# Optimization experiments

Measured on AMD Instinct MI355X. Metric: run time of the kernel, lower is better.

## Reference

```python
import jax, jax.numpy as jnp
import numpy as np
from jax import lax

B = 64            # batch size
IMG = 128         # image H=W
C_IN = 3          # channels (also conv kernel size in original code)
Q_DIM = 11
A_DIM = 10
CONV = [24, 24, 24, 24]
KS = 3
EPS = 1e-5
G_IN = (CONV[-1] + 2) * 2 + Q_DIM  # 63


def _lin_init(key, fin, fout):
    kw, kb = jax.random.split(key)
    w = jax.random.normal(kw, (fin, fout), jnp.float32) / np.sqrt(fin).astype(np.float32)
    b = jax.random.normal(kb, (fout,), jnp.float32) * 0.01
    return w, b


def _conv_init(key, cin, cout):
    kw, kb = jax.random.split(key)
    w = jax.random.normal(kw, (cout, cin, KS, KS), jnp.float32) / np.sqrt(cin * KS * KS).astype(np.float32)
    b = jax.random.normal(kb, (cout,), jnp.float32) * 0.01
    return w, b


def setup_inputs() -> dict:
    key = jax.random.key(0)
    ks = jax.random.split(key, 16)
    inp = {
        'img': jax.random.normal(ks[0], (B, C_IN, IMG, IMG), jnp.float32),
        'q': jax.random.normal(ks[1], (B, Q_DIM), jnp.float32),
    }
    cins = [C_IN] + CONV[:-1]
    for li in range(4):
        w, b = _conv_init(ks[2 + li], cins[li], CONV[li])
        inp[f'cw{li+1}'], inp[f'cb{li+1}'] = w, b
        inp[f'bg{li+1}'] = jnp.ones((CONV[li],), jnp.float32)
        inp[f'bb{li+1}'] = jnp.zeros((CONV[li],), jnp.float32)
    gins = [G_IN, 256, 256, 256]
    for li in range(4):
        w, b = _lin_init(ks[6 + li], gins[li], 256)
        inp[f'gw{li+1}'], inp[f'gb{li+1}'] = w, b
    fins, fouts = [256, 256, 256], [256, 256, A_DIM]
    for li in range(3):
        w, b = _lin_init(ks[10 + li], fins[li], fouts[li])
        inp[f'fw{li+1}'], inp[f'fb{li+1}'] = w, b
    return inp


def _conv_block(x, w, b, g, bb):
    # conv(stride=2, pad=1) -> relu -> batchnorm (train-mode batch stats)
    x = lax.conv_general_dilated(x, w, (2, 2), [(1, 1), (1, 1)],
                                 dimension_numbers=('NCHW', 'OIHW', 'NCHW'))
    x = jax.nn.relu(x + b[None, :, None, None])
    m = jnp.mean(x, axis=(0, 2, 3), keepdims=True)
    v = jnp.var(x, axis=(0, 2, 3), keepdims=True)
    return g[None, :, None, None] * (x - m) * jax.lax.rsqrt(v + EPS) + bb[None, :, None, None]


def _forward(img, q,
             cw1, cb1, bg1, bb1, cw2, cb2, bg2, bb2,
             cw3, cb3, bg3, bb3, cw4, cb4, bg4, bb4,
             gw1, gb1, gw2, gb2, gw3, gb3, gw4, gb4,
             fw1, fb1, fw2, fb2, fw3, fb3):
    x = _conv_block(img, cw1, cb1, bg1, bb1)
    x = _conv_block(x, cw2, cb2, bg2, bb2)
    x = _conv_block(x, cw3, cb3, bg3, bb3)
    x = _conv_block(x, cw4, cb4, bg4, bb4)        # [B, K, d, d]
    d = x.shape[2]
    N = d * d
    Kc = x.shape[1]
    # objects: o at flat index i corresponds to pixel (i//d, i%d) -> row-major reshape
    objs = x.reshape(B, Kc, N).transpose(0, 2, 1)           # [B, N, K]
    idx = jnp.arange(N)
    coords = jnp.stack([(idx // d).astype(jnp.float32) / d,
                        (idx % d).astype(jnp.float32) / d], axis=1)  # [N, 2]
    o = jnp.concatenate([objs, jnp.broadcast_to(coords[None], (B, N, 2))], axis=-1)  # [B, N, K+2]
    F = Kc + 2
    oi = jnp.broadcast_to(o[:, :, None, :], (B, N, N, F))
    oj = jnp.broadcast_to(o[:, None, :, :], (B, N, N, F))
    qb = jnp.broadcast_to(q[:, None, None, :], (B, N, N, Q_DIM))
    pair = jnp.concatenate([oi, oj, qb], axis=-1)           # [B, N, N, 2F+Q]
    h = jax.nn.relu(jnp.einsum('bijf,fh->bijh', pair, gw1) + gb1)
    h = jax.nn.relu(h @ gw2 + gb2)
    h = jax.nn.relu(h @ gw3 + gb3)
    h = jax.nn.relu(h @ gw4 + gb4)
    g = jnp.mean(h, axis=(1, 2))                            # mean over all N*N pairs -> [B, 256]
    # f_phi (dropout as identity / eval mode)
    g = jax.nn.relu(g @ fw1 + fb1)
    g = jax.nn.relu(g @ fw2 + fb2)
    logits = g @ fw3 + fb3
    return logits


def reference(img, q,
              cw1, cb1, bg1, bb1, cw2, cb2, bg2, bb2,
              cw3, cb3, bg3, bb3, cw4, cb4, bg4, bb4,
              gw1, gb1, gw2, gb2, gw3, gb3, gw4, gb4,
              fw1, fb1, fw2, fb2, fw3, fb3):
    return _forward(img, q,
                    cw1, cb1, bg1, bb1, cw2, cb2, bg2, bb2,
                    cw3, cb3, bg3, bb3, cw4, cb4, bg4, bb4,
                    gw1, gb1, gw2, gb2, gw3, gb3, gw4, gb4,
                    fw1, fb1, fw2, fb2, fw3, fb3)
```

## Files before the change

kernel.cpp:

```cpp
#include <hip/hip_runtime.h>
#include <hip/hip_bf16.h>

#define EPS_BN 1e-5f

typedef __bf16 bf16_t;
typedef __bf16 bf16x8 __attribute__((ext_vector_type(8)));
typedef __bf16 bf16x4 __attribute__((ext_vector_type(4)));
typedef float fx4 __attribute__((ext_vector_type(4)));
typedef float floatx16 __attribute__((ext_vector_type(16)));

__global__ __launch_bounds__(256) void c1prep_kernel(
    const float* __restrict__ img, const float* __restrict__ w,
    const float* __restrict__ bias, float* __restrict__ out,
    float* __restrict__ part_out,
    const float* __restrict__ q, const float* __restrict__ gw1,
    const float* __restrict__ gb1, const float* __restrict__ g2,
    const float* __restrict__ g3, const float* __restrict__ g4,
    const float* __restrict__ gb2, const float* __restrict__ gb3,
    float* __restrict__ wq, bf16_t* __restrict__ wpack,
    float* __restrict__ biaspack)
{
    int t = threadIdx.x;
    if (blockIdx.x >= 2048) {
        int blk = blockIdx.x - 2048;
        {
            float acc = gb1[t];
            #pragma unroll
            for (int d = 0; d < 11; d++)
                acc = fmaf(q[blk * 11 + d], gw1[(52 + d) * 256 + t], acc);
            wq[blk * 256 + t] = acc;
        }
        if (blk == 0) {
            for (int idx = t; idx < 512; idx += 256) {
                int layer = idx >> 8;
                int rem = idx & 255;
                int cg = rem >> 5, l2 = (rem >> 4) & 1, reg = rem & 15;
                int c = cg * 32 + (reg & 3) + 8 * (reg >> 2) + 4 * l2;
                biaspack[idx] = (layer ? gb3 : gb2)[c];
            }
        }
        for (int f = blk * 384 + t; f < blk * 384 + 384; f += 256) {
            int lane = f & 63;
            int kt = (f >> 6) & 15;
            int cg = (f >> 10) & 7;
            int layer = f >> 13;
            const float* gw = (layer == 0) ? g2 : ((layer == 1) ? g3 : g4);
            int col = (cg << 5) + (lane & 31);
            int kb = kt * 16 + (lane >> 5) * 8;
            bf16x8 o;
            #pragma unroll
            for (int e = 0; e < 8; e++)
                o[e] = (bf16_t)gw[(kb + e) * 256 + col];
            *(bf16x8*)&wpack[(size_t)f * 8] = o;
        }
        return;
    }
    __shared__ float tin[3][7][130];
    __shared__ float red[4][24];
    int b = blockIdx.x / 32, tile = blockIdx.x % 32;
    int oy0 = tile * 2;
    int iyb = 2 * oy0 - 1;
    #pragma unroll 2
    for (int idx = t; idx < 3 * 7 * 130; idx += 256) {
        int rx = idx % 130;
        int rem = idx / 130;
        int ry = rem % 7;
        int ci = rem / 7;
        int iy = iyb + ry, ix = rx - 1;
        float v = 0.f;
        if ((unsigned)iy < 128u && (unsigned)ix < 128u)
            v = img[(b * 3 + ci) * 16384 + iy * 128 + ix];
        tin[ci][ry][rx] = v;
    }
    __syncthreads();
    int ox = t % 64;
    int oyl = (t / 64) % 2;
    int cog = t / 128;
    const float* wp = w + cog * 12 * 27;
    float acc[12];
    #pragma unroll
    for (int r = 0; r < 12; r++) acc[r] = bias[cog * 12 + r];
    #pragma unroll
    for (int ci = 0; ci < 3; ci++)
        #pragma unroll
        for (int ky = 0; ky < 3; ky++)
            #pragma unroll
            for (int kx = 0; kx < 3; kx++) {
                float v = tin[ci][2 * oyl + ky][2 * ox + kx];
                #pragma unroll
                for (int r = 0; r < 12; r++)
                    acc[r] = fmaf(v, wp[(r * 3 + ci) * 9 + ky * 3 + kx], acc[r]);
            }
    int oy = oy0 + oyl;
    float s1[12], s2[12];
    #pragma unroll
    for (int r = 0; r < 12; r++) {
        float v = fmaxf(acc[r], 0.f);
        out[((b * 24 + cog * 12 + r) * 64 + oy) * 64 + ox] = v;
        s1[r] = v;
        s2[r] = v * v;
    }
    int lane = t & 63, w_id = t >> 6;
    #pragma unroll
    for (int r = 0; r < 12; r++) {
        float a = s1[r], c2 = s2[r];
        #pragma unroll
        for (int off = 32; off > 0; off >>= 1) {
            a += __shfl_xor(a, off);
            c2 += __shfl_xor(c2, off);
        }
        if (lane == 0) { red[w_id][r * 2] = a; red[w_id][r * 2 + 1] = c2; }
    }
    __syncthreads();
    if (t < 48) {
        int ch = t >> 1, st = t & 1;
        int cg2 = ch / 12, r = ch % 12;
        part_out[blockIdx.x * 48 + t] = red[cg2 * 2][r * 2 + st] + red[cg2 * 2 + 1][r * 2 + st];
    }
}

__global__ __launch_bounds__(256) void fin_kernel(
    const float* __restrict__ part, int P, float inv_n,
    const float* __restrict__ gamma, const float* __restrict__ beta,
    float* __restrict__ scsh)
{
    int c = blockIdx.x;
    int t = threadIdx.x;
    float s1 = 0.f, s2 = 0.f;
    for (int p = t; p < P; p += 256) {
        s1 += part[p * 48 + 2 * c];
        s2 += part[p * 48 + 2 * c + 1];
    }
    #pragma unroll
    for (int off = 32; off > 0; off >>= 1) {
        s1 += __shfl_xor(s1, off);
        s2 += __shfl_xor(s2, off);
    }
    __shared__ float r1[4], r2[4];
    int lane = t & 63, w = t >> 6;
    if (lane == 0) { r1[w] = s1; r2[w] = s2; }
    __syncthreads();
    if (t == 0) {
        float a1 = r1[0] + r1[1] + r1[2] + r1[3];
        float a2 = r2[0] + r2[1] + r2[2] + r2[3];
        float m = a1 * inv_n;
        float var = a2 * inv_n - m * m;
        float sc = gamma[c] * rsqrtf(var + EPS_BN);
        scsh[c] = sc;
        scsh[24 + c] = fmaf(-m, sc, beta[c]);
    }
}

template<int CIN, int HOUT, int OY_PER, int CO_PER, int PSTAT>
__global__ __launch_bounds__(256) void conv_kernel(
    const float* __restrict__ in, const float* __restrict__ scsh_in,
    const float* __restrict__ part_in, float inv_n,
    const float* __restrict__ gamma, const float* __restrict__ beta,
    const float* __restrict__ w, const float* __restrict__ bias,
    float* __restrict__ out, float* __restrict__ part_out)
{
    const int HIN = 2 * HOUT, ROWS = 2 * OY_PER + 3, RW = 2 * HOUT + 2;
    const int TILES = HOUT / OY_PER;
    const int WPC = (HOUT * OY_PER) / 64;
    int b = blockIdx.x / TILES, tile = blockIdx.x % TILES;
    int oy0 = tile * OY_PER;
    __shared__ float tin[CIN][ROWS][RW];
    __shared__ float scf[24], shf[24];
    __shared__ float fred[5][48];
    __shared__ float red[4][CO_PER * 2];
    int t = threadIdx.x;
    if (PSTAT > 0) {
        if (t < 240) {
            int comp = t % 48, sl = t / 48;
            float a = 0.f;
            for (int p = sl; p < PSTAT; p += 5) a += part_in[p * 48 + comp];
            fred[sl][comp] = a;
        }
        __syncthreads();
        if (t < 24) {
            float s1 = 0.f, s2 = 0.f;
            #pragma unroll
            for (int s = 0; s < 5; s++) { s1 += fred[s][2 * t]; s2 += fred[s][2 * t + 1]; }
            float m = s1 * inv_n;
            float var = s2 * inv_n - m * m;
            float sc = gamma[t] * rsqrtf(var + EPS_BN);
            scf[t] = sc;
            shf[t] = fmaf(-m, sc, beta[t]);
        }
        __syncthreads();
    } else {
        if (t < 24) { scf[t] = scsh_in[t]; shf[t] = scsh_in[24 + t]; }
        __syncthreads();
    }
    const int total = CIN * ROWS * RW;
    int iyb = 2 * oy0 - 1;
    #pragma unroll 2
    for (int idx = t; idx < total; idx += 256) {
        int rx = idx % RW;
        int rem = idx / RW;
        int ry = rem % ROWS;
        int ci = rem / ROWS;
        int iy = iyb + ry, ix = rx - 1;
        float v = 0.f;
        if ((unsigned)iy < (unsigned)HIN && (unsigned)ix < (unsigned)HIN)
            v = fmaf(in[(b * CIN + ci) * HIN * HIN + iy * HIN + ix], scf[ci], shf[ci]);
        tin[ci][ry][rx] = v;
    }
    __syncthreads();
    int ox = t % HOUT;
    int oyl = (t / HOUT) % OY_PER;
    int cog = t / (HOUT * OY_PER);
    const float* wp = w + cog * CO_PER * CIN * 9;
    float acc[CO_PER];
    #pragma unroll
    for (int r = 0; r < CO_PER; r++) acc[r] = bias[cog * CO_PER + r];
    for (int ci = 0; ci < CIN; ci++)
        #pragma unroll
        for (int ky = 0; ky < 3; ky++)
            #pragma unroll
            for (int kx = 0; kx < 3; kx++) {
                float v = tin[ci][2 * oyl + ky][2 * ox + kx];
                #pragma unroll
                for (int r = 0; r < CO_PER; r++)
                    acc[r] = fmaf(v, wp[(r * CIN + ci) * 9 + ky * 3 + kx], acc[r]);
            }
    int oy = oy0 + oyl;
    float s1[CO_PER], s2[CO_PER];
    #pragma unroll
    for (int r = 0; r < CO_PER; r++) {
        float v = fmaxf(acc[r], 0.f);
        out[((b * 24 + cog * CO_PER + r) * HOUT + oy) * HOUT + ox] = v;
        s1[r] = v;
        s2[r] = v * v;
    }
    int lane = t & 63, w_id = t >> 6;
    #pragma unroll
    for (int r = 0; r < CO_PER; r++) {
        float a = s1[r], c2 = s2[r];
        #pragma unroll
        for (int off = 32; off > 0; off >>= 1) {
            a += __shfl_xor(a, off);
            c2 += __shfl_xor(c2, off);
        }
        if (lane == 0) { red[w_id][r * 2] = a; red[w_id][r * 2 + 1] = c2; }
    }
    __syncthreads();
    if (t < 48) {
        int ch = t >> 1, st = t & 1;
        int cg = ch / CO_PER, r = ch % CO_PER;
        float v = 0.f;
        #pragma unroll
        for (int k = 0; k < WPC; k++) v += red[cg * WPC + k][r * 2 + st];
        part_out[blockIdx.x * 48 + t] = v;
    }
}

__global__ __launch_bounds__(256) void uv_kernel(
    const float* __restrict__ x4, const float* __restrict__ p4,
    const float* __restrict__ g4, const float* __restrict__ b4,
    const float* __restrict__ gw1, float* __restrict__ U, float* __restrict__ V)
{
    int b = blockIdx.x >> 2, n0 = (blockIdx.x & 3) * 16;
    __shared__ float o[16][26];
    __shared__ float fred[5][48];
    __shared__ float scf[24], shf[24];
    int t = threadIdx.x;
    if (t < 240) {
        int comp = t % 48, sl = t / 48;
        float a = 0.f;
        for (int p = sl; p < 64; p += 5) a += p4[p * 48 + comp];
        fred[sl][comp] = a;
    }
    __syncthreads();
    if (t < 24) {
        float s1 = 0.f, s2 = 0.f;
        #pragma unroll
        for (int s = 0; s < 5; s++) { s1 += fred[s][2 * t]; s2 += fred[s][2 * t + 1]; }
        float m = s1 * (1.f / 4096.f);
        float var = s2 * (1.f / 4096.f) - m * m;
        float sc = g4[t] * rsqrtf(var + EPS_BN);
        scf[t] = sc;
        shf[t] = fmaf(-m, sc, b4[t]);
    }
    __syncthreads();
    for (int idx = t; idx < 16 * 26; idx += 256) {
        int n = idx / 26, f = idx % 26;
        int ng = n0 + n;
        float val;
        if (f < 24)
            val = fmaf(x4[(b * 24 + f) * 64 + ng], scf[f], shf[f]);
        else if (f == 24) val = (float)(ng >> 3) * 0.125f;
        else              val = (float)(ng & 7) * 0.125f;
        o[n][f] = val;
    }
    __syncthreads();
    float g1u[26], g1v[26];
    #pragma unroll
    for (int f = 0; f < 26; f++) {
        g1u[f] = gw1[f * 256 + t];
        g1v[f] = gw1[(26 + f) * 256 + t];
    }
    for (int n = 0; n < 16; n++) {
        float u = 0.f, v = 0.f;
        #pragma unroll
        for (int f = 0; f < 26; f++) {
            float of = o[n][f];
            u = fmaf(of, g1u[f], u);
            v = fmaf(of, g1v[f], v);
        }
        int ng = n0 + n;
        U[(b * 64 + ng) * 256 + t] = u;
        V[(b * 64 + ng) * 256 + t] = v;
    }
}

__global__ __launch_bounds__(256, 3) void pair_kernel(
    const float* __restrict__ U, const float* __restrict__ V,
    const float* __restrict__ wq, const bf16_t* __restrict__ wpack,
    const float* __restrict__ biaspack, const float* __restrict__ gb4,
    float* __restrict__ partial)
{
    __shared__ __align__(16) bf16_t hA[64][264];
    int blk = blockIdx.x;
    int b = blk >> 6;
    int i = blk & 63;
    int t = threadIdx.x;

    {
        int cc = t & 31, jg = t >> 5;
        int c0 = cc * 8;
        const float* Ub = U + (b * 64 + i) * 256 + c0;
        const float* Qb = wq + b * 256 + c0;
        fx4 u0 = *(const fx4*)Ub + *(const fx4*)Qb;
        fx4 u1 = *(const fx4*)(Ub + 4) + *(const fx4*)(Qb + 4);
        const float* Vb = V + (b * 64) * 256 + c0;
        #pragma unroll
        for (int r = 0; r < 8; r++) {
            int j = jg * 8 + r;
            const float* Vr = Vb + j * 256;
            fx4 v0 = *(const fx4*)Vr + u0;
            fx4 v1 = *(const fx4*)(Vr + 4) + u1;
            bf16x8 o;
            #pragma unroll
            for (int e = 0; e < 4; e++) {
                o[e]     = (bf16_t)fmaxf(v0[e], 0.f);
                o[e + 4] = (bf16_t)fmaxf(v1[e], 0.f);
            }
            *(bf16x8*)&hA[j][c0] = o;
        }
    }
    __syncthreads();

    int lane = t & 63, wave = t >> 6;
    int l31 = lane & 31, l2 = lane >> 5;
    const floatx16 zero16 = {0.f, 0.f, 0.f, 0.f, 0.f, 0.f, 0.f, 0.f,
                             0.f, 0.f, 0.f, 0.f, 0.f, 0.f, 0.f, 0.f};

    int cm = wave;
    #pragma unroll 1
    for (int lay = 0; lay < 2; lay++) {
        floatx16 acc[2][2];
        #pragma unroll
        for (int mt = 0; mt < 2; mt++)
            #pragma unroll
            for (int nt = 0; nt < 2; nt++) acc[mt][nt] = zero16;

        const bf16_t* W0 = wpack + ((size_t)(lay * 8 + cm * 2) * 1024 + lane) * 8;
        const bf16_t* W1 = W0 + 8192;
        bf16x8 Aq[4][2];
        #pragma unroll
        for (int p = 0; p < 4; p++) {
            Aq[p][0] = *(const bf16x8*)(W0 + p * 512);
            Aq[p][1] = *(const bf16x8*)(W1 + p * 512);
        }
        #pragma unroll
        for (int ks = 0; ks < 16; ks++) {
            int slot = ks & 3;
            bf16x8 a0 = Aq[slot][0];
            bf16x8 a1 = Aq[slot][1];
            if (ks < 12) {
                Aq[slot][0] = *(const bf16x8*)(W0 + (ks + 4) * 512);
                Aq[slot][1] = *(const bf16x8*)(W1 + (ks + 4) * 512);
            }
            bf16x8 b0 = *(const bf16x8*)&hA[l31][ks * 16 + l2 * 8];
            bf16x8 b1 = *(const bf16x8*)&hA[32 + l31][ks * 16 + l2 * 8];
            acc[0][0] = __builtin_amdgcn_mfma_f32_32x32x16_bf16(a0, b0, acc[0][0], 0, 0, 0);
            acc[0][1] = __builtin_amdgcn_mfma_f32_32x32x16_bf16(a0, b1, acc[0][1], 0, 0, 0);
            acc[1][0] = __builtin_amdgcn_mfma_f32_32x32x16_bf16(a1, b0, acc[1][0], 0, 0, 0);
            acc[1][1] = __builtin_amdgcn_mfma_f32_32x32x16_bf16(a1, b1, acc[1][1], 0, 0, 0);
        }
        __syncthreads();
        #pragma unroll
        for (int mt = 0; mt < 2; mt++) {
            const fx4* bp = (const fx4*)(biaspack + lay * 256 + (cm * 2 + mt) * 32 + l2 * 16);
            fx4 bv[4];
            #pragma unroll
            for (int g = 0; g < 4; g++) bv[g] = bp[g];
            int cb = cm * 64 + mt * 32 + 4 * l2;
            #pragma unroll
            for (int nt = 0; nt < 2; nt++) {
                int j = nt * 32 + l31;
                #pragma unroll
                for (int g = 0; g < 4; g++) {
                    bf16x4 o;
                    #pragma unroll
                    for (int r = 0; r < 4; r++)
                        o[r] = (bf16_t)fmaxf(acc[mt][nt][g * 4 + r] + bv[g][r], 0.f);
                    *(bf16x4*)&hA[j][cb + 8 * g] = o;
                }
            }
        }
        __syncthreads();
    }

    int cn = wave;
    {
        float bcol[2] = {gb4[cn * 64 + l31], gb4[cn * 64 + 32 + l31]};
        floatx16 acc[2][2];
        #pragma unroll
        for (int mt = 0; mt < 2; mt++)
            #pragma unroll
            for (int nt = 0; nt < 2; nt++) acc[mt][nt] = zero16;
        const bf16_t* B0 = wpack + ((size_t)(16 + cn * 2) * 1024 + lane) * 8;
        const bf16_t* B1 = B0 + 8192;
        bf16x8 Bq[4][2];
        #pragma unroll
        for (int p = 0; p < 4; p++) {
            Bq[p][0] = *(const bf16x8*)(B0 + p * 512);
            Bq[p][1] = *(const bf16x8*)(B1 + p * 512);
        }
        #pragma unroll
        for (int ks = 0; ks < 16; ks++) {
            int slot = ks & 3;
            bf16x8 w0 = Bq[slot][0];
            bf16x8 w1 = Bq[slot][1];
            if (ks < 12) {
                Bq[slot][0] = *(const bf16x8*)(B0 + (ks + 4) * 512);
                Bq[slot][1] = *(const bf16x8*)(B1 + (ks + 4) * 512);
            }
            bf16x8 a0 = *(const bf16x8*)&hA[l31][ks * 16 + l2 * 8];
            bf16x8 a1 = *(const bf16x8*)&hA[32 + l31][ks * 16 + l2 * 8];
            acc[0][0] = __builtin_amdgcn_mfma_f32_32x32x16_bf16(a0, w0, acc[0][0], 0, 0, 0);
            acc[1][0] = __builtin_amdgcn_mfma_f32_32x32x16_bf16(a1, w0, acc[1][0], 0, 0, 0);
            acc[0][1] = __builtin_amdgcn_mfma_f32_32x32x16_bf16(a0, w1, acc[0][1], 0, 0, 0);
            acc[1][1] = __builtin_amdgcn_mfma_f32_32x32x16_bf16(a1, w1, acc[1][1], 0, 0, 0);
        }
        float colsum[2];
        #pragma unroll
        for (int nt = 0; nt < 2; nt++) {
            float s = 0.f;
            #pragma unroll
            for (int mt = 0; mt < 2; mt++)
                #pragma unroll
                for (int reg = 0; reg < 16; reg++)
                    s += fmaxf(acc[mt][nt][reg] + bcol[nt], 0.0f);
            colsum[nt] = s;
        }
        #pragma unroll
        for (int nt = 0; nt < 2; nt++)
            colsum[nt] += __shfl_xor(colsum[nt], 32);
        if (l2 == 0) {
            #pragma unroll
            for (int nt = 0; nt < 2; nt++)
                partial[blk * 256 + cn * 64 + nt * 32 + l31] = colsum[nt];
        }
    }
}

__global__ __launch_bounds__(256) void fphi_kernel(
    const float* __restrict__ partial,
    const float* __restrict__ fw1, const float* __restrict__ fb1,
    const float* __restrict__ fw2, const float* __restrict__ fb2,
    const float* __restrict__ fw3, const float* __restrict__ fb3,
    float* __restrict__ out)
{
    int b = blockIdx.x, t = threadIdx.x;
    __shared__ float g[256], h1[256], h2[256];
    float s = 0.f;
    for (int k = 0; k < 64; k++) s += partial[(b * 64 + k) * 256 + t];
    g[t] = s * (1.0f / 4096.0f);
    __syncthreads();
    float a1 = fb1[t];
    for (int k = 0; k < 256; k++) a1 = fmaf(g[k], fw1[k * 256 + t], a1);
    h1[t] = fmaxf(a1, 0.0f);
    __syncthreads();
    float a2 = fb2[t];
    for (int k = 0; k < 256; k++) a2 = fmaf(h1[k], fw2[k * 256 + t], a2);
    h2[t] = fmaxf(a2, 0.0f);
    __syncthreads();
    if (t < 10) {
        float a3 = fb3[t];
        for (int k = 0; k < 256; k++) a3 = fmaf(h2[k], fw3[k * 10 + t], a3);
        out[b * 10 + t] = a3;
    }
}

extern "C" void kernel_launch(void* const* d_in, const int* in_sizes, int n_in,
                              void* d_out, int out_size, void* d_ws, size_t ws_size,
                              hipStream_t stream)
{
    (void)in_sizes; (void)n_in; (void)out_size; (void)ws_size;
    const float* img = (const float*)d_in[0];
    const float* q   = (const float*)d_in[1];
    const float* cw[4] = {(const float*)d_in[2],  (const float*)d_in[6],
                          (const float*)d_in[10], (const float*)d_in[14]};
    const float* cb[4] = {(const float*)d_in[3],  (const float*)d_in[7],
                          (const float*)d_in[11], (const float*)d_in[15]};
    const float* bg[4] = {(const float*)d_in[4],  (const float*)d_in[8],
                          (const float*)d_in[12], (const float*)d_in[16]};
    const float* bbv[4] = {(const float*)d_in[5],  (const float*)d_in[9],
                           (const float*)d_in[13], (const float*)d_in[17]};
    const float* gw1 = (const float*)d_in[18]; const float* gb1 = (const float*)d_in[19];
    const float* gw2 = (const float*)d_in[20]; const float* gb2 = (const float*)d_in[21];
    const float* gw3 = (const float*)d_in[22]; const float* gb3 = (const float*)d_in[23];
    const float* gw4 = (const float*)d_in[24]; const float* gb4 = (const float*)d_in[25];
    const float* fw1 = (const float*)d_in[26]; const float* fb1 = (const float*)d_in[27];
    const float* fw2 = (const float*)d_in[28]; const float* fb2 = (const float*)d_in[29];
    const float* fw3 = (const float*)d_in[30]; const float* fb3 = (const float*)d_in[31];

    float* ws  = (float*)d_ws;
    float* x1  = ws;
    float* x2  = x1 + 6291456;
    float* x3  = x2 + 1572864;
    float* x4  = x3 + 393216;
    float* U   = x4 + 98304;
    float* V   = U + 1048576;
    float* wqv = V + 1048576;
    float* part = wqv + 16384;
    float* p1  = part + 1048576;
    float* p2  = p1 + 98304;
    float* p3  = p2 + 49152;
    float* p4  = p3 + 12288;
    float* scsh1 = p4 + 3072;
    float* scsh2 = scsh1 + 48;
    float* biaspack = scsh2 + 48;
    bf16_t* wpack = (bf16_t*)(biaspack + 512);

    c1prep_kernel<<<2112, 256, 0, stream>>>(
        img, cw[0], cb[0], x1, p1,
        q, gw1, gb1, gw2, gw3, gw4, gb2, gb3, wqv, wpack, biaspack);
    fin_kernel<<<24, 256, 0, stream>>>(p1, 2048, 1.f / 262144.f, bg[0], bbv[0], scsh1);
    conv_kernel<24, 32, 2, 6, -1><<<1024, 256, 0, stream>>>(
        x1, scsh1, nullptr, 0.f, nullptr, nullptr, cw[1], cb[1], x2, p2);
    fin_kernel<<<24, 256, 0, stream>>>(p2, 1024, 1.f / 65536.f, bg[1], bbv[1], scsh2);
    conv_kernel<24, 16, 4, 6, -1><<<256, 256, 0, stream>>>(
        x2, scsh2, nullptr, 0.f, nullptr, nullptr, cw[2], cb[2], x3, p3);
    conv_kernel<24, 8, 8, 6, 256><<<64, 256, 0, stream>>>(
        x3, nullptr, p3, 1.f / 16384.f, bg[2], bbv[2], cw[3], cb[3], x4, p4);
    uv_kernel<<<256, 256, 0, stream>>>(x4, p4, bg[3], bbv[3], gw1, U, V);
    pair_kernel<<<4096, 256, 0, stream>>>(U, V, wqv, wpack, biaspack, gb4, part);
    fphi_kernel<<<64, 256, 0, stream>>>(part, fw1, fb1, fw2, fb2, fw3, fb3,
                                        (float*)d_out);
}
```

Before: 431.8 us.

## Fuse all stages into one cooperative persistent kernel with grid syncs

Replaces the chain of nine kernel launches with one cooperative mega-kernel that loops over work units per stage and separates stages with grid.sync(). It also retiles conv2/conv3 into 2D tiles (16x4) and makes conv4 read precomputed BN scale/shift. The intent is to remove launch gaps and the tail of small kernels. In exchange, grid size is capped by occupancy (at most 1024 blocks), shared memory is sized for the largest stage, and the pair stage, which was tuned for 3 blocks per CU, may lose occupancy and latency hiding. A multi-kernel fallback is kept for when the cooperative launch fails.

```diff
diff --git a/kernel.cpp b/kernel.cpp
--- a/kernel.cpp
+++ b/kernel.cpp
@@ -1,5 +1,8 @@
 #include <hip/hip_runtime.h>
 #include <hip/hip_bf16.h>
+#include <hip/hip_cooperative_groups.h>
+
+namespace cg = cooperative_groups;
 
 #define EPS_BN 1e-5f
 
@@ -9,207 +12,89 @@
 typedef float fx4 __attribute__((ext_vector_type(4)));
 typedef float floatx16 __attribute__((ext_vector_type(16)));
 
-__global__ __launch_bounds__(256) void c1prep_kernel(
-    const float* __restrict__ img, const float* __restrict__ w,
-    const float* __restrict__ bias, float* __restrict__ out,
-    float* __restrict__ part_out,
-    const float* __restrict__ q, const float* __restrict__ gw1,
-    const float* __restrict__ gb1, const float* __restrict__ g2,
-    const float* __restrict__ g3, const float* __restrict__ g4,
-    const float* __restrict__ gb2, const float* __restrict__ gb3,
-    float* __restrict__ wq, bf16_t* __restrict__ wpack,
-    float* __restrict__ biaspack)
-{
-    int t = threadIdx.x;
-    if (blockIdx.x >= 2048) {
-        int blk = blockIdx.x - 2048;
-        {
-            float acc = gb1[t];
-            #pragma unroll
-            for (int d = 0; d < 11; d++)
-                acc = fmaf(q[blk * 11 + d], gw1[(52 + d) * 256 + t], acc);
-            wq[blk * 256 + t] = acc;
-        }
-        if (blk == 0) {
-            for (int idx = t; idx < 512; idx += 256) {
-                int layer = idx >> 8;
-                int rem = idx & 255;
-                int cg = rem >> 5, l2 = (rem >> 4) & 1, reg = rem & 15;
-                int c = cg * 32 + (reg & 3) + 8 * (reg >> 2) + 4 * l2;
-                biaspack[idx] = (layer ? gb3 : gb2)[c];
-            }
-        }
-        for (int f = blk * 384 + t; f < blk * 384 + 384; f += 256) {
-            int lane = f & 63;
-            int kt = (f >> 6) & 15;
-            int cg = (f >> 10) & 7;
-            int layer = f >> 13;
-            const float* gw = (layer == 0) ? g2 : ((layer == 1) ? g3 : g4);
-            int col = (cg << 5) + (lane & 31);
-            int kb = kt * 16 + (lane >> 5) * 8;
-            bf16x8 o;
-            #pragma unroll
-            for (int e = 0; e < 8; e++)
-                o[e] = (bf16_t)gw[(kb + e) * 256 + col];
-            *(bf16x8*)&wpack[(size_t)f * 8] = o;
-        }
-        return;
-    }
-    __shared__ float tin[3][7][130];
-    __shared__ float red[4][24];
-    int b = blockIdx.x / 32, tile = blockIdx.x % 32;
-    int oy0 = tile * 2;
-    int iyb = 2 * oy0 - 1;
-    #pragma unroll 2
-    for (int idx = t; idx < 3 * 7 * 130; idx += 256) {
-        int rx = idx % 130;
-        int rem = idx / 130;
-        int ry = rem % 7;
-        int ci = rem / 7;
-        int iy = iyb + ry, ix = rx - 1;
-        float v = 0.f;
-        if ((unsigned)iy < 128u && (unsigned)ix < 128u)
-            v = img[(b * 3 + ci) * 16384 + iy * 128 + ix];
-        tin[ci][ry][rx] = v;
-    }
-    __syncthreads();
-    int ox = t % 64;
-    int oyl = (t / 64) % 2;
-    int cog = t / 128;
-    const float* wp = w + cog * 12 * 27;
-    float acc[12];
-    #pragma unroll
-    for (int r = 0; r < 12; r++) acc[r] = bias[cog * 12 + r];
-    #pragma unroll
-    for (int ci = 0; ci < 3; ci++)
-        #pragma unroll
-        for (int ky = 0; ky < 3; ky++)
-            #pragma unroll
-            for (int kx = 0; kx < 3; kx++) {
-                float v = tin[ci][2 * oyl + ky][2 * ox + kx];
-                #pragma unroll
-                for (int r = 0; r < 12; r++)
-                    acc[r] = fmaf(v, wp[(r * 3 + ci) * 9 + ky * 3 + kx], acc[r]);
-            }
-    int oy = oy0 + oyl;
-    float s1[12], s2[12];
-    #pragma unroll
-    for (int r = 0; r < 12; r++) {
-        float v = fmaxf(acc[r], 0.f);
-        out[((b * 24 + cog * 12 + r) * 64 + oy) * 64 + ox] = v;
-        s1[r] = v;
-        s2[r] = v * v;
-    }
-    int lane = t & 63, w_id = t >> 6;
-    #pragma unroll
-    for (int r = 0; r < 12; r++) {
-        float a = s1[r], c2 = s2[r];
-        #pragma unroll
-        for (int off = 32; off > 0; off >>= 1) {
-            a += __shfl_xor(a, off);
-            c2 += __shfl_xor(c2, off);
-        }
-        if (lane == 0) { red[w_id][r * 2] = a; red[w_id][r * 2 + 1] = c2; }
-    }
-    __syncthreads();
-    if (t < 48) {
-        int ch = t >> 1, st = t & 1;
-        int cg2 = ch / 12, r = ch % 12;
-        part_out[blockIdx.x * 48 + t] = red[cg2 * 2][r * 2 + st] + red[cg2 * 2 + 1][r * 2 + st];
-    }
-}
-
-__global__ __launch_bounds__(256) void fin_kernel(
-    const float* __restrict__ part, int P, float inv_n,
-    const float* __restrict__ gamma, const float* __restrict__ beta,
-    float* __restrict__ scsh)
-{
-    int c = blockIdx.x;
-    int t = threadIdx.x;
-    float s1 = 0.f, s2 = 0.f;
-    for (int p = t; p < P; p += 256) {
-        s1 += part[p * 48 + 2 * c];
-        s2 += part[p * 48 + 2 * c + 1];
-    }
-    #pragma unroll
-    for (int off = 32; off > 0; off >>= 1) {
-        s1 += __shfl_xor(s1, off);
-        s2 += __shfl_xor(s2, off);
-    }
-    __shared__ float r1[4], r2[4];
-    int lane = t & 63, w = t >> 6;
-    if (lane == 0) { r1[w] = s1; r2[w] = s2; }
-    __syncthreads();
-    if (t == 0) {
-        float a1 = r1[0] + r1[1] + r1[2] + r1[3];
-        float a2 = r2[0] + r2[1] + r2[2] + r2[3];
-        float m = a1 * inv_n;
-        float var = a2 * inv_n - m * m;
-        float sc = gamma[c] * rsqrtf(var + EPS_BN);
-        scsh[c] = sc;
-        scsh[24 + c] = fmaf(-m, sc, beta[c]);
-    }
-}
-
-template<int CIN, int HOUT, int OY_PER, int CO_PER, int PSTAT>
-__global__ __launch_bounds__(256) void conv_kernel(
-    const float* __restrict__ in, const float* __restrict__ scsh_in,
-    const float* __restrict__ part_in, float inv_n,
-    const float* __restrict__ gamma, const float* __restrict__ beta,
-    const float* __restrict__ w, const float* __restrict__ bias,
-    float* __restrict__ out, float* __restrict__ part_out)
-{
-    const int HIN = 2 * HOUT, ROWS = 2 * OY_PER + 3, RW = 2 * HOUT + 2;
-    const int TILES = HOUT / OY_PER;
-    const int WPC = (HOUT * OY_PER) / 64;
-    int b = blockIdx.x / TILES, tile = blockIdx.x % TILES;
-    int oy0 = tile * OY_PER;
-    __shared__ float tin[CIN][ROWS][RW];
-    __shared__ float scf[24], shf[24];
-    __shared__ float fred[5][48];
-    __shared__ float red[4][CO_PER * 2];
-    int t = threadIdx.x;
-    if (PSTAT > 0) {
-        if (t < 240) {
-            int comp = t % 48, sl = t / 48;
-            float a = 0.f;
-            for (int p = sl; p < PSTAT; p += 5) a += part_in[p * 48 + comp];
-            fred[sl][comp] = a;
-        }
-        __syncthreads();
-        if (t < 24) {
-            float s1 = 0.f, s2 = 0.f;
-            #pragma unroll
-            for (int s = 0; s < 5; s++) { s1 += fred[s][2 * t]; s2 += fred[s][2 * t + 1]; }
-            float m = s1 * inv_n;
-            float var = s2 * inv_n - m * m;
-            float sc = gamma[t] * rsqrtf(var + EPS_BN);
-            scf[t] = sc;
-            shf[t] = fmaf(-m, sc, beta[t]);
-        }
-        __syncthreads();
-    } else {
-        if (t < 24) { scf[t] = scsh_in[t]; shf[t] = scsh_in[24 + t]; }
-        __syncthreads();
-    }
+struct Params {
+    const float *img, *q;
+    const float *cw1, *cb1, *bg1, *bb1;
+    const float *cw2, *cb2, *bg2, *bb2;
+    const float *cw3, *cb3, *bg3, *bb3;
+    const float *cw4, *cb4, *bg4, *bb4;
+    const float *gw1, *gb1, *gw2, *gb2, *gw3, *gb3, *gw4, *gb4;
+    const float *fw1, *fb1, *fw2, *fb2, *fw3, *fb3;
+    float* out;
+    float *x1, *x2, *x3, *x4, *U, *V, *wq, *part;
+    float *p1, *p2, *p3, *p4, *scsh1, *scsh2, *scsh3, *biaspack;
+    bf16_t* wpack;
+};
+
+#define SFLOATS 8976
+
+__device__ __forceinline__ void prep_fn(const Params& p, int blk, int t)
+{
+    {
+        float acc = p.gb1[t];
+        #pragma unroll
+        for (int d = 0; d < 11; d++)
+            acc = fmaf(p.q[blk * 11 + d], p.gw1[(52 + d) * 256 + t], acc);
+        p.wq[blk * 256 + t] = acc;
+    }
+    if (blk == 0) {
+        for (int idx = t; idx < 512; idx += 256) {
+            int layer = idx >> 8;
+            int rem = idx & 255;
+            int cg2 = rem >> 5, l2 = (rem >> 4) & 1, reg = rem & 15;
+            int c = cg2 * 32 + (reg & 3) + 8 * (reg >> 2) + 4 * l2;
+            p.biaspack[idx] = (layer ? p.gb3 : p.gb2)[c];
+        }
+    }
+    for (int f = blk * 384 + t; f < blk * 384 + 384; f += 256) {
+        int lane = f & 63;
+        int kt = (f >> 6) & 15;
+        int cg2 = (f >> 10) & 7;
+        int layer = f >> 13;
+        const float* gw = (layer == 0) ? p.gw2 : ((layer == 1) ? p.gw3 : p.gw4);
+        int col = (cg2 << 5) + (lane & 31);
+        int kb = kt * 16 + (lane >> 5) * 8;
+        bf16x8 o;
+        #pragma unroll
+        for (int e = 0; e < 8; e++)
+            o[e] = (bf16_t)gw[(kb + e) * 256 + col];
+        *(bf16x8*)&p.wpack[(size_t)f * 8] = o;
+    }
+}
+
+template<int CIN, int HOUT, int TOX, int TOY, int CO_PER, bool FOLD>
+__device__ __forceinline__ void conv_tile(
+    float* tin, const float* scf, const float* shf, float (&red)[4][48],
+    const float* in, const float* w, const float* bias,
+    float* out, float* part_out, int u, int t)
+{
+    const int HIN = 2 * HOUT, ROWS = 2 * TOY + 3, RW = 2 * TOX + 2;
+    const int TX = HOUT / TOX, TY = HOUT / TOY;
+    const int WPC = (TOX * TOY) / 64;
+    int b = u / (TX * TY);
+    int rem = u % (TX * TY);
+    int ty = rem / TX, tx = rem % TX;
+    int oy0 = ty * TOY, ox0 = tx * TOX;
     const int total = CIN * ROWS * RW;
-    int iyb = 2 * oy0 - 1;
+    int iyb = 2 * oy0 - 1, ixb = 2 * ox0 - 1;
     #pragma unroll 2
     for (int idx = t; idx < total; idx += 256) {
         int rx = idx % RW;
-        int rem = idx / RW;
-        int ry = rem % ROWS;
-        int ci = rem / ROWS;
-        int iy = iyb + ry, ix = rx - 1;
+        int r2 = idx / RW;
+        int ry = r2 % ROWS;
+        int ci = r2 / ROWS;
+        int iy = iyb + ry, ix = ixb + rx;
         float v = 0.f;
-        if ((unsigned)iy < (unsigned)HIN && (unsigned)ix < (unsigned)HIN)
-            v = fmaf(in[(b * CIN + ci) * HIN * HIN + iy * HIN + ix], scf[ci], shf[ci]);
-        tin[ci][ry][rx] = v;
-    }
-    __syncthreads();
-    int ox = t % HOUT;
-    int oyl = (t / HOUT) % OY_PER;
-    int cog = t / (HOUT * OY_PER);
+        if ((unsigned)iy < (unsigned)HIN && (unsigned)ix < (unsigned)HIN) {
+            float raw = in[(b * CIN + ci) * HIN * HIN + iy * HIN + ix];
+            v = FOLD ? fmaf(raw, scf[ci], shf[ci]) : raw;
+        }
+        tin[(ci * ROWS + ry) * RW + rx] = v;
+    }
+    __syncthreads();
+    int ox = t % TOX;
+    int oyl = (t / TOX) % TOY;
+    int cog = t / (TOX * TOY);
     const float* wp = w + cog * CO_PER * CIN * 9;
     float acc[CO_PER];
     #pragma unroll
@@ -219,7 +104,7 @@
         for (int ky = 0; ky < 3; ky++)
             #pragma unroll
             for (int kx = 0; kx < 3; kx++) {
-                float v = tin[ci][2 * oyl + ky][2 * ox + kx];
+                float v = tin[(ci * ROWS + 2 * oyl + ky) * RW + 2 * ox + kx];
                 #pragma unroll
                 for (int r = 0; r < CO_PER; r++)
                     acc[r] = fmaf(v, wp[(r * CIN + ci) * 9 + ky * 3 + kx], acc[r]);
@@ -229,7 +114,7 @@
     #pragma unroll
     for (int r = 0; r < CO_PER; r++) {
         float v = fmaxf(acc[r], 0.f);
-        out[((b * 24 + cog * CO_PER + r) * HOUT + oy) * HOUT + ox] = v;
+        out[((b * 24 + cog * CO_PER + r) * HOUT + oy) * HOUT + ox0 + ox] = v;
         s1[r] = v;
         s2[r] = v * v;
     }
@@ -247,28 +132,53 @@
     __syncthreads();
     if (t < 48) {
         int ch = t >> 1, st = t & 1;
-        int cg = ch / CO_PER, r = ch % CO_PER;
+        int cg2 = ch / CO_PER, r = ch % CO_PER;
         float v = 0.f;
         #pragma unroll
-        for (int k = 0; k < WPC; k++) v += red[cg * WPC + k][r * 2 + st];
-        part_out[blockIdx.x * 48 + t] = v;
-    }
-}
-
-__global__ __launch_bounds__(256) void uv_kernel(
-    const float* __restrict__ x4, const float* __restrict__ p4,
-    const float* __restrict__ g4, const float* __restrict__ b4,
-    const float* __restrict__ gw1, float* __restrict__ U, float* __restrict__ V)
-{
-    int b = blockIdx.x >> 2, n0 = (blockIdx.x & 3) * 16;
-    __shared__ float o[16][26];
-    __shared__ float fred[5][48];
-    __shared__ float scf[24], shf[24];
-    int t = threadIdx.x;
+        for (int k = 0; k < WPC; k++) v += red[cg2 * WPC + k][r * 2 + st];
+        part_out[u * 48 + t] = v;
+    }
+    __syncthreads();
+}
+
+__device__ __forceinline__ void fin_fn(
+    const float* part, int Pn, float inv_n, const float* gamma,
+    const float* beta, float* scsh, float (&red)[4][48], int c, int t)
+{
+    float s1 = 0.f, s2 = 0.f;
+    for (int pr = t; pr < Pn; pr += 256) {
+        s1 += part[pr * 48 + 2 * c];
+        s2 += part[pr * 48 + 2 * c + 1];
+    }
+    #pragma unroll
+    for (int off = 32; off > 0; off >>= 1) {
+        s1 += __shfl_xor(s1, off);
+        s2 += __shfl_xor(s2, off);
+    }
+    int lane = t & 63, w = t >> 6;
+    if (lane == 0) { red[w][0] = s1; red[w][1] = s2; }
+    __syncthreads();
+    if (t == 0) {
+        float a1 = red[0][0] + red[1][0] + red[2][0] + red[3][0];
+        float a2 = red[0][1] + red[1][1] + red[2][1] + red[3][1];
+        float m = a1 * inv_n;
+        float var = a2 * inv_n - m * m;
+        float sc = gamma[c] * rsqrtf(var + EPS_BN);
+        scsh[c] = sc;
+        scsh[24 + c] = fmaf(-m, sc, beta[c]);
+    }
+    __syncthreads();
+}
+
+__device__ __forceinline__ void uv_fn(
+    float* o, float (&fred)[5][48], float* scf, float* shf,
+    const Params& p, int u, int t)
+{
+    int b = u >> 2, n0 = (u & 3) * 16;
     if (t < 240) {
         int comp = t % 48, sl = t / 48;
         float a = 0.f;
-        for (int p = sl; p < 64; p += 5) a += p4[p * 48 + comp];
+        for (int pr = sl; pr < 64; pr += 5) a += p.p4[pr * 48 + comp];
         fred[sl][comp] = a;
     }
     __syncthreads();
@@ -278,9 +188,9 @@
         for (int s = 0; s < 5; s++) { s1 += fred[s][2 * t]; s2 += fred[s][2 * t + 1]; }
         float m = s1 * (1.f / 4096.f);
         float var = s2 * (1.f / 4096.f) - m * m;
-        float sc = g4[t] * rsqrtf(var + EPS_BN);
+        float sc = p.bg4[t] * rsqrtf(var + EPS_BN);
         scf[t] = sc;
-        shf[t] = fmaf(-m, sc, b4[t]);
+        shf[t] = fmaf(-m, sc, p.bb4[t]);
     }
     __syncthreads();
     for (int idx = t; idx < 16 * 26; idx += 256) {
@@ -288,52 +198,45 @@
         int ng = n0 + n;
         float val;
         if (f < 24)
-            val = fmaf(x4[(b * 24 + f) * 64 + ng], scf[f], shf[f]);
+            val = fmaf(p.x4[(b * 24 + f) * 64 + ng], scf[f], shf[f]);
         else if (f == 24) val = (float)(ng >> 3) * 0.125f;
         else              val = (float)(ng & 7) * 0.125f;
-        o[n][f] = val;
+        o[n * 26 + f] = val;
     }
     __syncthreads();
     float g1u[26], g1v[26];
     #pragma unroll
     for (int f = 0; f < 26; f++) {
-        g1u[f] = gw1[f * 256 + t];
-        g1v[f] = gw1[(26 + f) * 256 + t];
+        g1u[f] = p.gw1[f * 256 + t];
+        g1v[f] = p.gw1[(26 + f) * 256 + t];
     }
     for (int n = 0; n < 16; n++) {
-        float u = 0.f, v = 0.f;
+        float uu = 0.f, vv = 0.f;
         #pragma unroll
         for (int f = 0; f < 26; f++) {
-            float of = o[n][f];
-            u = fmaf(of, g1u[f], u);
-            v = fmaf(of, g1v[f], v);
+            float of = o[n * 26 + f];
+            uu = fmaf(of, g1u[f], uu);
+            vv = fmaf(of, g1v[f], vv);
         }
         int ng = n0 + n;
-        U[(b * 64 + ng) * 256 + t] = u;
-        V[(b * 64 + ng) * 256 + t] = v;
-    }
-}
-
-__global__ __launch_bounds__(256, 3) void pair_kernel(
-    const float* __restrict__ U, const float* __restrict__ V,
-    const float* __restrict__ wq, const bf16_t* __restrict__ wpack,
-    const float* __restrict__ biaspack, const float* __restrict__ gb4,
-    float* __restrict__ partial)
-{
-    __shared__ __align__(16) bf16_t hA[64][264];
-    int blk = blockIdx.x;
-    int b = blk >> 6;
-    int i = blk & 63;
-    int t = threadIdx.x;
-
+        p.U[(b * 64 + ng) * 256 + t] = uu;
+        p.V[(b * 64 + ng) * 256 + t] = vv;
+    }
+    __syncthreads();
+}
+
+__device__ __forceinline__ void pair_fn(bf16_t* hA, const Params& p, int u, int t)
+{
+    int b = u >> 6, i = u & 63;
+    __syncthreads();
     {
         int cc = t & 31, jg = t >> 5;
         int c0 = cc * 8;
-        const float* Ub = U + (b * 64 + i) * 256 + c0;
-        const float* Qb = wq + b * 256 + c0;
+        const float* Ub = p.U + (b * 64 + i) * 256 + c0;
+        const float* Qb = p.wq + b * 256 + c0;
         fx4 u0 = *(const fx4*)Ub + *(const fx4*)Qb;
         fx4 u1 = *(const fx4*)(Ub + 4) + *(const fx4*)(Qb + 4);
-        const float* Vb = V + (b * 64) * 256 + c0;
+        const float* Vb = p.V + (b * 64) * 256 + c0;
         #pragma unroll
         for (int r = 0; r < 8; r++) {
             int j = jg * 8 + r;
@@ -346,7 +249,7 @@
                 o[e]     = (bf16_t)fmaxf(v0[e], 0.f);
                 o[e + 4] = (bf16_t)fmaxf(v1[e], 0.f);
             }
-            *(bf16x8*)&hA[j][c0] = o;
+            *(bf16x8*)&hA[j * 264 + c0] = o;
         }
     }
     __syncthreads();
@@ -364,14 +267,13 @@
         for (int mt = 0; mt < 2; mt++)
             #pragma unroll
             for (int nt = 0; nt < 2; nt++) acc[mt][nt] = zero16;
-
-        const bf16_t* W0 = wpack + ((size_t)(lay * 8 + cm * 2) * 1024 + lane) * 8;
+        const bf16_t* W0 = p.wpack + ((size_t)(lay * 8 + cm * 2) * 1024 + lane) * 8;
         const bf16_t* W1 = W0 + 8192;
         bf16x8 Aq[4][2];
         #pragma unroll
-        for (int p = 0; p < 4; p++) {
-            Aq[p][0] = *(const bf16x8*)(W0 + p * 512);
-            Aq[p][1] = *(const bf16x8*)(W1 + p * 512);
+        for (int pr = 0; pr < 4; pr++) {
+            Aq[pr][0] = *(const bf16x8*)(W0 + pr * 512);
+            Aq[pr][1] = *(const bf16x8*)(W1 + pr * 512);
         }
         #pragma unroll
         for (int ks = 0; ks < 16; ks++) {
@@ -382,8 +284,8 @@
                 Aq[slot][0] = *(const bf16x8*)(W0 + (ks + 4) * 512);
                 Aq[slot][1] = *(const bf16x8*)(W1 + (ks + 4) * 512);
             }
-            bf16x8 b0 = *(const bf16x8*)&hA[l31][ks * 16 + l2 * 8];
-            bf16x8 b1 = *(const bf16x8*)&hA[32 + l31][ks * 16 + l2 * 8];
+            bf16x8 b0 = *(const bf16x8*)&hA[l31 * 264 + ks * 16 + l2 * 8];
+            bf16x8 b1 = *(const bf16x8*)&hA[(32 + l31) * 264 + ks * 16 + l2 * 8];
             acc[0][0] = __builtin_amdgcn_mfma_f32_32x32x16_bf16(a0, b0, acc[0][0], 0, 0, 0);
             acc[0][1] = __builtin_amdgcn_mfma_f32_32x32x16_bf16(a0, b1, acc[0][1], 0, 0, 0);
             acc[1][0] = __builtin_amdgcn_mfma_f32_32x32x16_bf16(a1, b0, acc[1][0], 0, 0, 0);
@@ -392,7 +294,7 @@
         __syncthreads();
         #pragma unroll
         for (int mt = 0; mt < 2; mt++) {
-            const fx4* bp = (const fx4*)(biaspack + lay * 256 + (cm * 2 + mt) * 32 + l2 * 16);
+            const fx4* bp = (const fx4*)(p.biaspack + lay * 256 + (cm * 2 + mt) * 32 + l2 * 16);
             fx4 bv[4];
             #pragma unroll
             for (int g = 0; g < 4; g++) bv[g] = bp[g];
@@ -406,7 +308,7 @@
                     #pragma unroll
                     for (int r = 0; r < 4; r++)
                         o[r] = (bf16_t)fmaxf(acc[mt][nt][g * 4 + r] + bv[g][r], 0.f);
-                    *(bf16x4*)&hA[j][cb + 8 * g] = o;
+                    *(bf16x4*)&hA[j * 264 + cb + 8 * g] = o;
                 }
             }
         }
@@ -415,19 +317,19 @@
 
     int cn = wave;
     {
-        float bcol[2] = {gb4[cn * 64 + l31], gb4[cn * 64 + 32 + l31]};
+        float bcol[2] = {p.gb4[cn * 64 + l31], p.gb4[cn * 64 + 32 + l31]};
         floatx16 acc[2][2];
         #pragma unroll
         for (int mt = 0; mt < 2; mt++)
             #pragma unroll
             for (int nt = 0; nt < 2; nt++) acc[mt][nt] = zero16;
-        const bf16_t* B0 = wpack + ((size_t)(16 + cn * 2) * 1024 + lane) * 8;
+        const bf16_t* B0 = p.wpack + ((size_t)(16 + cn * 2) * 1024 + lane) * 8;
         const bf16_t* B1 = B0 + 8192;
         bf16x8 Bq[4][2];
         #pragma unroll
-        for (int p = 0; p < 4; p++) {
-            Bq[p][0] = *(const bf16x8*)(B0 + p * 512);
-            Bq[p][1] = *(const bf16x8*)(B1 + p * 512);
+        for (int pr = 0; pr < 4; pr++) {
+            Bq[pr][0] = *(const bf16x8*)(B0 + pr * 512);
+            Bq[pr][1] = *(const bf16x8*)(B1 + pr * 512);
         }
         #pragma unroll
         for (int ks = 0; ks < 16; ks++) {
@@ -438,8 +340,8 @@
                 Bq[slot][0] = *(const bf16x8*)(B0 + (ks + 4) * 512);
                 Bq[slot][1] = *(const bf16x8*)(B1 + (ks + 4) * 512);
             }
-            bf16x8 a0 = *(const bf16x8*)&hA[l31][ks * 16 + l2 * 8];
-            bf16x8 a1 = *(const bf16x8*)&hA[32 + l31][ks * 16 + l2 * 8];
+            bf16x8 a0 = *(const bf16x8*)&hA[l31 * 264 + ks * 16 + l2 * 8];
+            bf16x8 a1 = *(const bf16x8*)&hA[(32 + l31) * 264 + ks * 16 + l2 * 8];
             acc[0][0] = __builtin_amdgcn_mfma_f32_32x32x16_bf16(a0, w0, acc[0][0], 0, 0, 0);
             acc[1][0] = __builtin_amdgcn_mfma_f32_32x32x16_bf16(a1, w0, acc[1][0], 0, 0, 0);
             acc[0][1] = __builtin_amdgcn_mfma_f32_32x32x16_bf16(a0, w1, acc[0][1], 0, 0, 0);
@@ -462,37 +364,139 @@
         if (l2 == 0) {
             #pragma unroll
             for (int nt = 0; nt < 2; nt++)
-                partial[blk * 256 + cn * 64 + nt * 32 + l31] = colsum[nt];
-        }
-    }
-}
-
-__global__ __launch_bounds__(256) void fphi_kernel(
-    const float* __restrict__ partial,
-    const float* __restrict__ fw1, const float* __restrict__ fb1,
-    const float* __restrict__ fw2, const float* __restrict__ fb2,
-    const float* __restrict__ fw3, const float* __restrict__ fb3,
-    float* __restrict__ out)
-{
-    int b = blockIdx.x, t = threadIdx.x;
-    __shared__ float g[256], h1[256], h2[256];
+                p.part[u * 256 + cn * 64 + nt * 32 + l31] = colsum[nt];
+        }
+    }
+}
+
+__device__ __forceinline__ void fphi_fn(float* ff, const Params& p, int b, int t)
+{
+    float* g  = ff;
+    float* h1 = ff + 256;
+    float* h2 = ff + 512;
+    __syncthreads();
     float s = 0.f;
-    for (int k = 0; k < 64; k++) s += partial[(b * 64 + k) * 256 + t];
+    for (int k = 0; k < 64; k++) s += p.part[(b * 64 + k) * 256 + t];
     g[t] = s * (1.0f / 4096.0f);
     __syncthreads();
-    float a1 = fb1[t];
-    for (int k = 0; k < 256; k++) a1 = fmaf(g[k], fw1[k * 256 + t], a1);
+    float a1 = p.fb1[t];
+    for (int k = 0; k < 256; k++) a1 = fmaf(g[k], p.fw1[k * 256 + t], a1);
     h1[t] = fmaxf(a1, 0.0f);
     __syncthreads();
-    float a2 = fb2[t];
-    for (int k = 0; k < 256; k++) a2 = fmaf(h1[k], fw2[k * 256 + t], a2);
+    float a2 = p.fb2[t];
+    for (int k = 0; k < 256; k++) a2 = fmaf(h1[k], p.fw2[k * 256 + t], a2);
     h2[t] = fmaxf(a2, 0.0f);
     __syncthreads();
     if (t < 10) {
-        float a3 = fb3[t];
-        for (int k = 0; k < 256; k++) a3 = fmaf(h2[k], fw3[k * 10 + t], a3);
-        out[b * 10 + t] = a3;
-    }
+        float a3 = p.fb3[t];
+        for (int k = 0; k < 256; k++) a3 = fmaf(h2[k], p.fw3[k * 10 + t], a3);
+        p.out[b * 10 + t] = a3;
+    }
+}
+
+__global__ __launch_bounds__(256, 4) void mega_kernel(Params p)
+{
+    __shared__ __align__(16) float S[SFLOATS];
+    __shared__ float scf[24], shf[24];
+    __shared__ float red[4][48];
+    __shared__ float fred[5][48];
+    cg::grid_group grid = cg::this_grid();
+    const int blk = blockIdx.x, t = threadIdx.x, G = gridDim.x;
+
+    for (int u = blk; u < 2048; u += G)
+        conv_tile<3, 64, 64, 2, 12, false>(S, scf, shf, red,
+            p.img, p.cw1, p.cb1, p.x1, p.p1, u, t);
+    if (blk < 64) prep_fn(p, blk, t);
+    grid.sync();
+    if (blk < 24) fin_fn(p.p1, 2048, 1.f / 262144.f, p.bg1, p.bb1, p.scsh1, red, blk, t);
+    grid.sync();
+
+    if (t < 24) { scf[t] = p.scsh1[t]; shf[t] = p.scsh1[24 + t]; }
+    __syncthreads();
+    for (int u = blk; u < 1024; u += G)
+        conv_tile<24, 32, 16, 4, 6, true>(S, scf, shf, red,
+            p.x1, p.cw2, p.cb2, p.x2, p.p2, u, t);
+    grid.sync();
+    if (blk < 24) fin_fn(p.p2, 1024, 1.f / 65536.f, p.bg2, p.bb2, p.scsh2, red, blk, t);
+    grid.sync();
+
+    if (t < 24) { scf[t] = p.scsh2[t]; shf[t] = p.scsh2[24 + t]; }
+    __syncthreads();
+    for (int u = blk; u < 256; u += G)
+        conv_tile<24, 16, 16, 4, 6, true>(S, scf, shf, red,
+            p.x2, p.cw3, p.cb3, p.x3, p.p3, u, t);
+    grid.sync();
+    if (blk < 24) fin_fn(p.p3, 256, 1.f / 16384.f, p.bg3, p.bb3, p.scsh3, red, blk, t);
+    grid.sync();
+
+    if (t < 24) { scf[t] = p.scsh3[t]; shf[t] = p.scsh3[24 + t]; }
+    __syncthreads();
+    for (int u = blk; u < 64; u += G)
+        conv_tile<24, 8, 8, 8, 6, true>(S, scf, shf, red,
+            p.x3, p.cw4, p.cb4, p.x4, p.p4, u, t);
+    grid.sync();
+
+    for (int u = blk; u < 256; u += G) uv_fn(S, fred, scf, shf, p, u, t);
+    grid.sync();
+
+    for (int u = blk; u < 4096; u += G) pair_fn((bf16_t*)S, p, u, t);
+    grid.sync();
+
+    for (int u = blk; u < 64; u += G) fphi_fn(S, p, u, t);
+}
+
+__global__ __launch_bounds__(256) void fb_c1prep(Params p)
+{
+    __shared__ __align__(16) float S[SFLOATS];
+    __shared__ float scf[24], shf[24];
+    __shared__ float red[4][48];
+    int t = threadIdx.x;
+    if (blockIdx.x >= 2048) { prep_fn(p, blockIdx.x - 2048, t); return; }
+    conv_tile<3, 64, 64, 2, 12, false>(S, scf, shf, red,
+        p.img, p.cw1, p.cb1, p.x1, p.p1, blockIdx.x, t);
+}
+
+__global__ __launch_bounds__(256) void fb_fin(
+    const float* part, int Pn, float inv_n, const float* gamma,
+    const float* beta, float* scsh)
+{
+    __shared__ float red[4][48];
+    fin_fn(part, Pn, inv_n, gamma, beta, scsh, red, blockIdx.x, threadIdx.x);
+}
+
+template<int CIN, int HOUT, int TOX, int TOY, int CO_PER>
+__global__ __launch_bounds__(256) void fb_conv(
+    const float* in, const float* scsh, const float* w, const float* bias,
+    float* out, float* part_out)
+{
+    __shared__ __align__(16) float S[SFLOATS];
+    __shared__ float scf[24], shf[24];
+    __shared__ float red[4][48];
+    int t = threadIdx.x;
+    if (t < 24) { scf[t] = scsh[t]; shf[t] = scsh[24 + t]; }
+    __syncthreads();
+    conv_tile<CIN, HOUT, TOX, TOY, CO_PER, true>(S, scf, shf, red,
+        in, w, bias, out, part_out, blockIdx.x, t);
+}
+
+__global__ __launch_bounds__(256) void fb_uv(Params p)
+{
+    __shared__ __align__(16) float S[SFLOATS];
+    __shared__ float scf[24], shf[24];
+    __shared__ float fred[5][48];
+    uv_fn(S, fred, scf, shf, p, blockIdx.x, threadIdx.x);
+}
+
+__global__ __launch_bounds__(256, 3) void fb_pair(Params p)
+{
+    __shared__ __align__(16) bf16_t hA[64 * 264];
+    pair_fn(hA, p, blockIdx.x, threadIdx.x);
+}
+
+__global__ __launch_bounds__(256) void fb_fphi(Params p)
+{
+    __shared__ __align__(16) float ff[768];
+    fphi_fn(ff, p, blockIdx.x, threadIdx.x);
 }
 
 extern "C" void kernel_launch(void* const* d_in, const int* in_sizes, int n_in,
@@ -500,55 +504,74 @@
                               hipStream_t stream)
 {
     (void)in_sizes; (void)n_in; (void)out_size; (void)ws_size;
-    const float* img = (const float*)d_in[0];
-    const float* q   = (const float*)d_in[1];
-    const float* cw[4] = {(const float*)d_in[2],  (const float*)d_in[6],
-                          (const float*)d_in[10], (const float*)d_in[14]};
-    const float* cb[4] = {(const float*)d_in[3],  (const float*)d_in[7],
-                          (const float*)d_in[11], (const float*)d_in[15]};
-    const float* bg[4] = {(const float*)d_in[4],  (const float*)d_in[8],
-                          (const float*)d_in[12], (const float*)d_in[16]};
-    const float* bbv[4] = {(const float*)d_in[5],  (const float*)d_in[9],
-                           (const float*)d_in[13], (const float*)d_in[17]};
-    const float* gw1 = (const float*)d_in[18]; const float* gb1 = (const float*)d_in[19];
-    const float* gw2 = (const float*)d_in[20]; const float* gb2 = (const float*)d_in[21];
-    const float* gw3 = (const float*)d_in[22]; const float* gb3 = (const float*)d_in[23];
-    const float* gw4 = (const float*)d_in[24]; const float* gb4 = (const float*)d_in[25];
-    const float* fw1 = (const float*)d_in[26]; const float* fb1 = (const float*)d_in[27];
-    const float* fw2 = (const float*)d_in[28]; const float* fb2 = (const float*)d_in[29];
-    const float* fw3 = (const float*)d_in[30]; const float* fb3 = (const float*)d_in[31];
-
-    float* ws  = (float*)d_ws;
-    float* x1  = ws;
-    float* x2  = x1 + 6291456;
-    float* x3  = x2 + 1572864;
-    float* x4  = x3 + 393216;
-    float* U   = x4 + 98304;
-    float* V   = U + 1048576;
-    float* wqv = V + 1048576;
-    float* part = wqv + 16384;
-    float* p1  = part + 1048576;
-    float* p2  = p1 + 98304;
-    float* p3  = p2 + 49152;
-    float* p4  = p3 + 12288;
-    float* scsh1 = p4 + 3072;
-    float* scsh2 = scsh1 + 48;
-    float* biaspack = scsh2 + 48;
-    bf16_t* wpack = (bf16_t*)(biaspack + 512);
-
-    c1prep_kernel<<<2112, 256, 0, stream>>>(
-        img, cw[0], cb[0], x1, p1,
-        q, gw1, gb1, gw2, gw3, gw4, gb2, gb3, wqv, wpack, biaspack);
-    fin_kernel<<<24, 256, 0, stream>>>(p1, 2048, 1.f / 262144.f, bg[0], bbv[0], scsh1);
-    conv_kernel<24, 32, 2, 6, -1><<<1024, 256, 0, stream>>>(
-        x1, scsh1, nullptr, 0.f, nullptr, nullptr, cw[1], cb[1], x2, p2);
-    fin_kernel<<<24, 256, 0, stream>>>(p2, 1024, 1.f / 65536.f, bg[1], bbv[1], scsh2);
-    conv_kernel<24, 16, 4, 6, -1><<<256, 256, 0, stream>>>(
-        x2, scsh2, nullptr, 0.f, nullptr, nullptr, cw[2], cb[2], x3, p3);
-    conv_kernel<24, 8, 8, 6, 256><<<64, 256, 0, stream>>>(
-        x3, nullptr, p3, 1.f / 16384.f, bg[2], bbv[2], cw[3], cb[3], x4, p4);
-    uv_kernel<<<256, 256, 0, stream>>>(x4, p4, bg[3], bbv[3], gw1, U, V);
-    pair_kernel<<<4096, 256, 0, stream>>>(U, V, wqv, wpack, biaspack, gb4, part);
-    fphi_kernel<<<64, 256, 0, stream>>>(part, fw1, fb1, fw2, fb2, fw3, fb3,
-                                        (float*)d_out);
-}
+    float* ws = (float*)d_ws;
+    Params p;
+    p.img = (const float*)d_in[0];
+    p.q   = (const float*)d_in[1];
+    p.cw1 = (const float*)d_in[2];  p.cb1 = (const float*)d_in[3];
+    p.bg1 = (const float*)d_in[4];  p.bb1 = (const float*)d_in[5];
+    p.cw2 = (const float*)d_in[6];  p.cb2 = (const float*)d_in[7];
+    p.bg2 = (const float*)d_in[8];  p.bb2 = (const float*)d_in[9];
+    p.cw3 = (const float*)d_in[10]; p.cb3 = (const float*)d_in[11];
+    p.bg3 = (const float*)d_in[12]; p.bb3 = (const float*)d_in[13];
+    p.cw4 = (const float*)d_in[14]; p.cb4 = (const float*)d_in[15];
+    p.bg4 = (const float*)d_in[16]; p.bb4 = (const float*)d_in[17];
+    p.gw1 = (const float*)d_in[18]; p.gb1 = (const float*)d_in[19];
+    p.gw2 = (const float*)d_in[20]; p.gb2 = (const float*)d_in[21];
+    p.gw3 = (const float*)d_in[22]; p.gb3 = (const float*)d_in[23];
+    p.gw4 = (const float*)d_in[24]; p.gb4 = (const float*)d_in[25];
+    p.fw1 = (const float*)d_in[26]; p.fb1 = (const float*)d_in[27];
+    p.fw2 = (const float*)d_in[28]; p.fb2 = (const float*)d_in[29];
+    p.fw3 = (const float*)d_in[30]; p.fb3 = (const float*)d_in[31];
+    p.out = (float*)d_out;
+
+    p.x1 = ws;
+    p.x2 = p.x1 + 6291456;
+    p.x3 = p.x2 + 1572864;
+    p.x4 = p.x3 + 393216;
+    p.U  = p.x4 + 98304;
+    p.V  = p.U + 1048576;
+    p.wq = p.V + 1048576;
+    p.part = p.wq + 16384;
+    p.p1 = p.part + 1048576;
+    p.p2 = p.p1 + 98304;
+    p.p3 = p.p2 + 49152;
+    p.p4 = p.p3 + 12288;
+    p.scsh1 = p.p4 + 3072;
+    p.scsh2 = p.scsh1 + 48;
+    p.scsh3 = p.scsh2 + 48;
+    p.biaspack = p.scsh3 + 48;
+    p.wpack = (bf16_t*)(p.biaspack + 512);
+
+    hipError_t e = hipErrorUnknown;
+    int dev = 0;
+    if (hipGetDevice(&dev) == hipSuccess) {
+        int numCU = 0, maxB = 0;
+        hipDeviceGetAttribute(&numCU, hipDeviceAttributeMultiprocessorCount, dev);
+        hipError_t qe = hipOccupancyMaxActiveBlocksPerMultiprocessor(
+            &maxB, mega_kernel, 256, 0);
+        long G = (qe == hipSuccess && numCU > 0) ? (long)numCU * maxB : 0;
+        if (G > 1024) G = 1024;
+        if (G >= 64) {
+            void* args[] = { &p };
+            e = hipLaunchCooperativeKernel((const void*)mega_kernel,
+                                           dim3((unsigned)G), dim3(256),
+                                           args, 0, stream);
+        }
+    }
+    if (e != hipSuccess) {
+        fb_c1prep<<<2112, 256, 0, stream>>>(p);
+        fb_fin<<<24, 256, 0, stream>>>(p.p1, 2048, 1.f / 262144.f, p.bg1, p.bb1, p.scsh1);
+        fb_conv<24, 32, 16, 4, 6><<<1024, 256, 0, stream>>>(
+            p.x1, p.scsh1, p.cw2, p.cb2, p.x2, p.p2);
+        fb_fin<<<24, 256, 0, stream>>>(p.p2, 1024, 1.f / 65536.f, p.bg2, p.bb2, p.scsh2);
+        fb_conv<24, 16, 16, 4, 6><<<256, 256, 0, stream>>>(
+            p.x2, p.scsh2, p.cw3, p.cb3, p.x3, p.p3);
+        fb_fin<<<24, 256, 0, stream>>>(p.p3, 256, 1.f / 16384.f, p.bg3, p.bb3, p.scsh3);
+        fb_conv<24, 8, 8, 8, 6><<<64, 256, 0, stream>>>(
+            p.x3, p.scsh3, p.cw4, p.cb4, p.x4, p.p4);
+        fb_uv<<<256, 256, 0, stream>>>(p);
+        fb_pair<<<4096, 256, 0, stream>>>(p);
+        fb_fphi<<<64, 256, 0, stream>>>(p);
+    }
+}
```

New measurement: 1.143 ms. 2.65x slower.
